# Kernel optimization log

Hardware: AMD Instinct MI355X
Metric: run time of the kernel (lower is better)

## Reference

```python
import jax, jax.numpy as jnp
import numpy as np

N, IN_DIM, H, D = 4096, 512, 8, 64
NEG = -1e9  # additive mask value for non-edges


def setup_inputs() -> dict:
    key = jax.random.key(0)
    k1, k2, k3, k4, k5, k6 = jax.random.split(key, 6)
    data = jax.random.normal(k1, (N, IN_DIM), dtype=jnp.float32)
    r = jax.random.uniform(k2, (N, N), dtype=jnp.float32)
    connectivity = jnp.where(r < 0.05, 0.0, NEG).astype(jnp.float32)
    # xavier-uniform-ish init for params
    lim_w = float(np.sqrt(6.0 / (IN_DIM + H * D)))
    W = jax.random.uniform(k3, (H * D, IN_DIM), jnp.float32, -lim_w, lim_w)
    b = jnp.zeros((H * D,), jnp.float32)
    lim_p = float(np.sqrt(6.0 / (H * D + 1)))
    src_proj = jax.random.uniform(k4, (1, H, D), jnp.float32, -lim_p, lim_p)
    trg_proj = jax.random.uniform(k5, (1, H, D), jnp.float32, -lim_p, lim_p)
    return {"data": data, "connectivity": connectivity, "W": W, "b": b,
            "src_proj": src_proj, "trg_proj": trg_proj}


def reference(data, connectivity, W, b, src_proj, trg_proj):
    # dropout is identity in eval mode (reference is deterministic)
    data1 = (data @ W.T + b).reshape(N, H, D)          # (N,H,D)
    src = jnp.einsum('nhd,xhd->nh', data1, src_proj)   # (N,H)
    trg = jnp.einsum('nhd,xhd->nh', data1, trg_proj)   # (N,H)
    # scores: (H,N,1) + (H,1,N) broadcast outer-sum
    e = src.T[:, :, None] + trg.T[:, None, :]          # (H,N,N)
    e = jnp.where(e >= 0, e, 0.01 * e)                 # LeakyReLU(0.01)
    e = e + connectivity[None, :, :]                   # additive mask
    scores = jax.nn.softmax(e, axis=-1)                # (H,N,N)
    # bmm over heads: (H,N,N) x (H,N,D) -> (H,N,D)
    out = jnp.einsum('hnm,hmd->hnd', scores, data1.transpose(1, 0, 2))
    out = out.transpose(1, 0, 2).reshape(N, H * D)     # concat=True
    return out
```

## Files before the change

kernel.cpp:

```cpp
#include <hip/hip_runtime.h>
#include <hip/hip_bf16.h>

#define NN 4096
#define IN_DIM 512
#define NH 8
#define DD 64
#define HD 512
#define LOG2E 1.4426950408889634f
#define CAST_WGS 2304
#define SCAN_WGS 1024


typedef __attribute__((ext_vector_type(8))) short short8;
typedef __attribute__((ext_vector_type(4))) float f32x4;

static __device__ __forceinline__ unsigned short f2bf(float x) {
    __hip_bfloat16 h = __float2bfloat16(x);
    return *reinterpret_cast<unsigned short*>(&h);
}

static __device__ __forceinline__ unsigned cvtpk_bf16(float a, float b) {
    unsigned r;
    asm("v_cvt_pk_bf16_f32 %0, %1, %2" : "=v"(r) : "v"(a), "v"(b));
    return r;
}

__global__ __launch_bounds__(256) void k_cast_scan(const float* __restrict__ inA,
                                                   unsigned short* __restrict__ outA,
                                                   int n4A,
                                                   const float* __restrict__ inB,
                                                   unsigned short* __restrict__ outB,
                                                   int n4B,
                                                   const float* __restrict__ conn,
                                                   unsigned long long* __restrict__ bm) {
    if (blockIdx.x >= CAST_WGS) {
        const int lane = threadIdx.x & 63;
        const int w = threadIdx.x >> 6;
        const int row = (blockIdx.x - CAST_WGS) * 4 + w;
        const float* crow = conn + (size_t)row * NN;
        unsigned long long keep = 0;
#pragma unroll 8
        for (int t = 0; t < 64; t++) {
            float c = crow[t * 64 + lane];
            unsigned long long m = __ballot(c == 0.0f);
            if (lane == t) keep = m;
        }
        bm[(size_t)row * 64 + lane] = keep;
        return;
    }
    int t = blockIdx.x * 256 + threadIdx.x;
    const float* in;
    unsigned short* out;
    if (t < n4A) {
        in = inA; out = outA;
    } else {
        t -= n4A;
        if (t >= n4B) return;
        in = inB; out = outB;
    }
    float4 v = ((const float4*)in)[t];
    ushort4 o;
    o.x = f2bf(v.x); o.y = f2bf(v.y); o.z = f2bf(v.z); o.w = f2bf(v.w);
    ((ushort4*)out)[t] = o;
}

__global__ __launch_bounds__(256) void k_gemm_fused(const unsigned short* __restrict__ Ab,
                                                    const unsigned short* __restrict__ Wb,
                                                    const float* __restrict__ bias,
                                                    const float* __restrict__ sp,
                                                    const float* __restrict__ tp,
                                                    unsigned short* __restrict__ d1t,
                                                    float* __restrict__ srcT,
                                                    float* __restrict__ trgT) {
    const int lane = threadIdx.x & 63;
    const int w = threadIdx.x >> 6;
    const int col = lane & 15;
    const int quad = lane >> 4;
    const int koff = quad * 8;
    const int h = blockIdx.x;
    const int m0 = h * 64;
    const int n0 = blockIdx.y * 64;

    const short8* ap  = (const short8*)(Ab + (size_t)(n0 + w * 16 + col) * IN_DIM + koff);
    const short8* bp0 = (const short8*)(Wb + (size_t)(m0 +  0 + col) * IN_DIM + koff);
    const short8* bp1 = (const short8*)(Wb + (size_t)(m0 + 16 + col) * IN_DIM + koff);
    const short8* bp2 = (const short8*)(Wb + (size_t)(m0 + 32 + col) * IN_DIM + koff);
    const short8* bp3 = (const short8*)(Wb + (size_t)(m0 + 48 + col) * IN_DIM + koff);

    f32x4 acc0 = {0.f, 0.f, 0.f, 0.f}, acc1 = acc0, acc2 = acc0, acc3 = acc0;

#pragma unroll 4
    for (int ks = 0; ks < 16; ks++) {
        short8 a  = ap[ks * 4];
        short8 b0 = bp0[ks * 4];
        short8 b1 = bp1[ks * 4];
        short8 b2 = bp2[ks * 4];
        short8 b3 = bp3[ks * 4];
        acc0 = __builtin_amdgcn_mfma_f32_16x16x32_bf16(a, b0, acc0, 0, 0, 0);
        acc1 = __builtin_amdgcn_mfma_f32_16x16x32_bf16(a, b1, acc1, 0, 0, 0);
        acc2 = __builtin_amdgcn_mfma_f32_16x16x32_bf16(a, b2, acc2, 0, 0, 0);
        acc3 = __builtin_amdgcn_mfma_f32_16x16x32_bf16(a, b3, acc3, 0, 0, 0);
    }

    const int rbase = n0 + w * 16 + quad * 4;
    const int jt  = (n0 >> 5) + (w >> 1);
    const int kqf = ((w & 1) << 1) + (quad >> 1);
    const int half = quad & 1;
    f32x4 accs[4] = {acc0, acc1, acc2, acc3};
    float ps[4] = {0.f, 0.f, 0.f, 0.f};
    float pt[4] = {0.f, 0.f, 0.f, 0.f};
#pragma unroll
    for (int mt = 0; mt < 4; mt++) {
        const int m = m0 + mt * 16 + col;
        const float bv  = bias[m];
        const float spv = sp[m];
        const float tpv = tp[m];
        ushort4 pack;
        unsigned short* pk = (unsigned short*)&pack;
#pragma unroll
        for (int r = 0; r < 4; r++) {
            float v = accs[mt][r] + bv;
            pk[r] = f2bf(v);
            ps[r] += v * spv;
            pt[r] += v * tpv;
        }
        size_t boff = ((((size_t)(h * 128 + jt) * 4 + mt) * 64 + kqf * 16 + col) << 4)
                    + ((size_t)half << 3);
        *(ushort4*)((char*)d1t + boff) = pack;
    }
#pragma unroll
    for (int off = 1; off <= 8; off <<= 1) {
#pragma unroll
        for (int r = 0; r < 4; r++) {
            ps[r] += __shfl_xor(ps[r], off, 64);
            pt[r] += __shfl_xor(pt[r], off, 64);
        }
    }
    if (col < 4)
        srcT[(size_t)h * NN + rbase + col] = ps[col] * LOG2E;
    else if (col < 8)
        trgT[(size_t)h * NN + rbase + col - 4] = pt[col - 4] * LOG2E;
}

__global__ __launch_bounds__(256) void k_flash(const unsigned* __restrict__ bm32,
                                               const float* __restrict__ srcT,
                                               const float* __restrict__ trgT,
                                               const unsigned short* __restrict__ d1t,
                                               float* __restrict__ out) {
    __shared__ char vt[2][16384];

    const int t = threadIdx.x;
    const int lane = t & 63;
    const int w = t >> 6;
    const int col = lane & 15;
    const int kq = lane >> 4;
    const int i0 = blockIdx.x * 64;
    const int h = blockIdx.y;
    const int m = i0 + w * 16 + col;

    const float s = srcT[(size_t)h * NN + m];
    const unsigned* bp = bm32 + (size_t)m * 128;
    const float* tpp = trgT + (size_t)h * NN + kq * 8;
    const uint4* gfrag = (const uint4*)d1t + (((size_t)h * 128) * 4 + w) * 64 + lane;
    const short8 ONES = {0x3F80, 0x3F80, 0x3F80, 0x3F80, 0x3F80, 0x3F80, 0x3F80, 0x3F80};

    f32x4 acc0 = {0.f, 0.f, 0.f, 0.f}, acc1 = acc0, acc2 = acc0, acc3 = acc0;
    f32x4 asum = acc0;

#pragma unroll
    for (int i = 0; i < 4; i++) {
        uint4 st = gfrag[(size_t)i * 256];
        *(uint4*)(vt[0] + ((i * 4 + w) * 64 + lane) * 16) = st;
    }
    __syncthreads();

    for (int step = 0; step < 32; step++) {
        const int cur = step & 1;
        uint4 bq = *(const uint4*)(bp + step * 4);
        float4 tA[4], tB[4];
#pragma unroll
        for (int jtl = 0; jtl < 4; jtl++) {
            tA[jtl] = *(const float4*)(tpp + (step * 4 + jtl) * 32);
            tB[jtl] = *(const float4*)(tpp + (step * 4 + jtl) * 32 + 4);
        }
        uint4 st0, st1, st2, st3;
        if (step < 31) {
            const uint4* gs = gfrag + (size_t)(step + 1) * 4 * 256;
            st0 = gs[0]; st1 = gs[256]; st2 = gs[512]; st3 = gs[768];
        }
        const unsigned bqa[4] = {bq.x, bq.y, bq.z, bq.w};

#pragma unroll
        for (int jtl = 0; jtl < 4; jtl++) {
            const unsigned bits = (bqa[jtl] >> (kq * 8)) & 0xffu;
            const float tv[8] = {tA[jtl].x, tA[jtl].y, tA[jtl].z, tA[jtl].w,
                                 tB[jtl].x, tB[jtl].y, tB[jtl].z, tB[jtl].w};
            float p[8];
#pragma unroll
            for (int r = 0; r < 8; r++) {
                float e = s + tv[r];
                e = fmaxf(e, 0.01f * e);
                float pv = __builtin_amdgcn_exp2f(e);
                pv *= (float)((bits >> r) & 1u);
                p[r] = pv;
            }
            union { uint4 u; short8 s8; } pk;
            pk.u.x = cvtpk_bf16(p[0], p[1]);
            pk.u.y = cvtpk_bf16(p[2], p[3]);
            pk.u.z = cvtpk_bf16(p[4], p[5]);
            pk.u.w = cvtpk_bf16(p[6], p[7]);
            const char* cb = vt[cur] + (jtl * 4 * 64) * 16 + lane * 16;
            short8 v0 = *(const short8*)(cb);
            short8 v1 = *(const short8*)(cb + 1024);
            short8 v2 = *(const short8*)(cb + 2048);
            short8 v3 = *(const short8*)(cb + 3072);
            acc0 = __builtin_amdgcn_mfma_f32_16x16x32_bf16(pk.s8, v0, acc0, 0, 0, 0);
            acc1 = __builtin_amdgcn_mfma_f32_16x16x32_bf16(pk.s8, v1, acc1, 0, 0, 0);
            acc2 = __builtin_amdgcn_mfma_f32_16x16x32_bf16(pk.s8, v2, acc2, 0, 0, 0);
            acc3 = __builtin_amdgcn_mfma_f32_16x16x32_bf16(pk.s8, v3, acc3, 0, 0, 0);
            asum = __builtin_amdgcn_mfma_f32_16x16x32_bf16(pk.s8, ONES, asum, 0, 0, 0);
        }

        if (step < 31) {
            char* wbuf = vt[cur ^ 1];
            *(uint4*)(wbuf + ((0 * 4 + w) * 64 + lane) * 16) = st0;
            *(uint4*)(wbuf + ((1 * 4 + w) * 64 + lane) * 16) = st1;
            *(uint4*)(wbuf + ((2 * 4 + w) * 64 + lane) * 16) = st2;
            *(uint4*)(wbuf + ((3 * 4 + w) * 64 + lane) * 16) = st3;
        }
        __syncthreads();
    }

    f32x4 accs[4] = {acc0, acc1, acc2, acc3};
#pragma unroll
    for (int r = 0; r < 4; r++) {
        const int row = i0 + w * 16 + kq * 4 + r;
        const float dv = asum[r];
        const float inv = (dv > 0.f) ? (1.f / dv) : 0.f;
        float* op = out + (size_t)row * HD + h * 64;
#pragma unroll
        for (int dt = 0; dt < 4; dt++)
            op[dt * 16 + col] = accs[dt][r] * inv;
    }
}

extern "C" void kernel_launch(void* const* d_in, const int* in_sizes, int n_in,
                              void* d_out, int out_size, void* d_ws, size_t ws_size,
                              hipStream_t stream) {
    const float* data = (const float*)d_in[0];
    const float* conn = (const float*)d_in[1];
    const float* W    = (const float*)d_in[2];
    const float* bias = (const float*)d_in[3];
    const float* sp   = (const float*)d_in[4];
    const float* tp   = (const float*)d_in[5];
    float* out = (float*)d_out;

    unsigned short* d1t = (unsigned short*)d_ws;
    unsigned short* Ab  = d1t + (size_t)HD * NN;
    unsigned short* Wb  = Ab + (size_t)NN * IN_DIM;
    float* srcT = (float*)(Wb + (size_t)HD * IN_DIM);
    float* trgT = srcT + NH * NN;
    unsigned long long* bm = (unsigned long long*)(trgT + NH * NN);

    const int n4A = NN * IN_DIM / 4;
    const int n4B = HD * IN_DIM / 4;
    k_cast_scan<<<dim3(CAST_WGS + SCAN_WGS), 256, 0, stream>>>(data, Ab, n4A, W, Wb, n4B,
                                                               conn, bm);
    k_gemm_fused<<<dim3(NH, NN / 64), 256, 0, stream>>>(Ab, Wb, bias, sp, tp,
                                                        d1t, srcT, trgT);
    k_flash<<<dim3(64, NH), 256, 0, stream>>>((const unsigned*)bm, srcT, trgT, d1t, out);
}
```

Before: 187.4 us.

## Widen flash attention block to 128 rows and prefetch two steps ahead

The flash kernel now runs 512 threads (8 waves) per block covering 128 query rows, so each V tile staged in shared memory is reused by twice as many waves and global V traffic per row is halved. The V tile load is spread across all 512 threads with contiguous indexing. Mask bits, target scores and V fragments are now software-pipelined two steps ahead, with register double-buffering and the shared-memory write moved to the start of each step. The trade-offs are a grid of only 256 blocks, which may leave less room for scheduling across CUs, and higher register pressure from the extra prefetch buffers under a 512-thread launch bound.

```diff
diff --git a/kernel.cpp b/kernel.cpp
--- a/kernel.cpp
+++ b/kernel.cpp
@@ -142,7 +142,7 @@
         trgT[(size_t)h * NN + rbase + col - 4] = pt[col - 4] * LOG2E;
 }
 
-__global__ __launch_bounds__(256) void k_flash(const unsigned* __restrict__ bm32,
+__global__ __launch_bounds__(512) void k_flash(const unsigned* __restrict__ bm32,
                                                const float* __restrict__ srcT,
                                                const float* __restrict__ trgT,
                                                const unsigned short* __restrict__ d1t,
@@ -154,47 +154,55 @@
     const int w = t >> 6;
     const int col = lane & 15;
     const int kq = lane >> 4;
-    const int i0 = blockIdx.x * 64;
+    const int i0 = blockIdx.x * 128;
     const int h = blockIdx.y;
     const int m = i0 + w * 16 + col;
 
     const float s = srcT[(size_t)h * NN + m];
     const unsigned* bp = bm32 + (size_t)m * 128;
     const float* tpp = trgT + (size_t)h * NN + kq * 8;
-    const uint4* gfrag = (const uint4*)d1t + (((size_t)h * 128) * 4 + w) * 64 + lane;
+    const uint4* gv = (const uint4*)d1t + (size_t)h * 32768;
     const short8 ONES = {0x3F80, 0x3F80, 0x3F80, 0x3F80, 0x3F80, 0x3F80, 0x3F80, 0x3F80};
 
     f32x4 acc0 = {0.f, 0.f, 0.f, 0.f}, acc1 = acc0, acc2 = acc0, acc3 = acc0;
     f32x4 asum = acc0;
 
-#pragma unroll
-    for (int i = 0; i < 4; i++) {
-        uint4 st = gfrag[(size_t)i * 256];
-        *(uint4*)(vt[0] + ((i * 4 + w) * 64 + lane) * 16) = st;
+    {
+        uint4 a0 = gv[t];
+        uint4 a1 = gv[t + 512];
+        *(uint4*)(vt[0] + (size_t)t * 16) = a0;
+        *(uint4*)(vt[0] + (size_t)(t + 512) * 16) = a1;
+    }
+    uint4 st0 = gv[1024 + t];
+    uint4 st1 = gv[1024 + t + 512];
+    uint4 bq_c = *(const uint4*)(bp);
+    uint4 bq_n = *(const uint4*)(bp + 4);
+    float4 tAc[4], tBc[4], tAn[4], tBn[4];
+#pragma unroll
+    for (int jtl = 0; jtl < 4; jtl++) {
+        tAc[jtl] = *(const float4*)(tpp + jtl * 32);
+        tBc[jtl] = *(const float4*)(tpp + jtl * 32 + 4);
+        tAn[jtl] = *(const float4*)(tpp + (4 + jtl) * 32);
+        tBn[jtl] = *(const float4*)(tpp + (4 + jtl) * 32 + 4);
     }
     __syncthreads();
 
+#pragma unroll 2
     for (int step = 0; step < 32; step++) {
         const int cur = step & 1;
-        uint4 bq = *(const uint4*)(bp + step * 4);
-        float4 tA[4], tB[4];
-#pragma unroll
-        for (int jtl = 0; jtl < 4; jtl++) {
-            tA[jtl] = *(const float4*)(tpp + (step * 4 + jtl) * 32);
-            tB[jtl] = *(const float4*)(tpp + (step * 4 + jtl) * 32 + 4);
-        }
-        uint4 st0, st1, st2, st3;
-        if (step < 31) {
-            const uint4* gs = gfrag + (size_t)(step + 1) * 4 * 256;
-            st0 = gs[0]; st1 = gs[256]; st2 = gs[512]; st3 = gs[768];
-        }
-        const unsigned bqa[4] = {bq.x, bq.y, bq.z, bq.w};
-
+        char* wb = vt[cur ^ 1];
+        *(uint4*)(wb + (size_t)t * 16) = st0;
+        *(uint4*)(wb + (size_t)(t + 512) * 16) = st1;
+        const int s2 = (step + 2 < 32) ? step + 2 : 31;
+        st0 = gv[s2 * 1024 + t];
+        st1 = gv[s2 * 1024 + t + 512];
+
+        const unsigned bqa[4] = {bq_c.x, bq_c.y, bq_c.z, bq_c.w};
 #pragma unroll
         for (int jtl = 0; jtl < 4; jtl++) {
             const unsigned bits = (bqa[jtl] >> (kq * 8)) & 0xffu;
-            const float tv[8] = {tA[jtl].x, tA[jtl].y, tA[jtl].z, tA[jtl].w,
-                                 tB[jtl].x, tB[jtl].y, tB[jtl].z, tB[jtl].w};
+            const float tv[8] = {tAc[jtl].x, tAc[jtl].y, tAc[jtl].z, tAc[jtl].w,
+                                 tBc[jtl].x, tBc[jtl].y, tBc[jtl].z, tBc[jtl].w};
             float p[8];
 #pragma unroll
             for (int r = 0; r < 8; r++) {
@@ -209,7 +217,7 @@
             pk.u.y = cvtpk_bf16(p[2], p[3]);
             pk.u.z = cvtpk_bf16(p[4], p[5]);
             pk.u.w = cvtpk_bf16(p[6], p[7]);
-            const char* cb = vt[cur] + (jtl * 4 * 64) * 16 + lane * 16;
+            const char* cb = vt[cur] + jtl * 4096 + lane * 16;
             short8 v0 = *(const short8*)(cb);
             short8 v1 = *(const short8*)(cb + 1024);
             short8 v2 = *(const short8*)(cb + 2048);
@@ -221,12 +229,14 @@
             asum = __builtin_amdgcn_mfma_f32_16x16x32_bf16(pk.s8, ONES, asum, 0, 0, 0);
         }
 
-        if (step < 31) {
-            char* wbuf = vt[cur ^ 1];
-            *(uint4*)(wbuf + ((0 * 4 + w) * 64 + lane) * 16) = st0;
-            *(uint4*)(wbuf + ((1 * 4 + w) * 64 + lane) * 16) = st1;
-            *(uint4*)(wbuf + ((2 * 4 + w) * 64 + lane) * 16) = st2;
-            *(uint4*)(wbuf + ((3 * 4 + w) * 64 + lane) * 16) = st3;
+        bq_c = bq_n;
+#pragma unroll
+        for (int jtl = 0; jtl < 4; jtl++) { tAc[jtl] = tAn[jtl]; tBc[jtl] = tBn[jtl]; }
+        bq_n = *(const uint4*)(bp + s2 * 4);
+#pragma unroll
+        for (int jtl = 0; jtl < 4; jtl++) {
+            tAn[jtl] = *(const float4*)(tpp + (s2 * 4 + jtl) * 32);
+            tBn[jtl] = *(const float4*)(tpp + (s2 * 4 + jtl) * 32 + 4);
         }
         __syncthreads();
     }
@@ -268,5 +278,5 @@
                                                                conn, bm);
     k_gemm_fused<<<dim3(NH, NN / 64), 256, 0, stream>>>(Ab, Wb, bias, sp, tp,
                                                         d1t, srcT, trgT);
-    k_flash<<<dim3(64, NH), 256, 0, stream>>>((const unsigned*)bm, srcT, trgT, d1t, out);
-}
+    k_flash<<<dim3(NN / 128, NH), 512, 0, stream>>>((const unsigned*)bm, srcT, trgT, d1t, out);
+}
```

After: 184.3 us. Within noise of the previous version (-1.7%).
